# Kernel optimization log

Hardware: AMD Instinct MI355X
Metric: run time of the kernel (lower is better)

## Reference

```python
import jax, jax.numpy as jnp
import numpy as np

DIM, N_HEADS, HEAD_DIM, BASE = 1024, 16, 64, 10000.0
B, S = 2, 2048


def setup_inputs() -> dict:
    key = jax.random.key(0)
    ks = jax.random.split(key, 8)
    theta = (BASE ** (-jnp.arange(0, HEAD_DIM, 2, dtype=jnp.float32) / HEAD_DIM))  # [head_dim//2]
    s = 0.02
    return {
        "x": jax.random.normal(ks[0], (B, S, DIM), jnp.float32),
        "positions": jnp.arange(S, dtype=jnp.int32),
        "theta": theta,
        "Wq": jax.random.normal(ks[1], (DIM, N_HEADS * HEAD_DIM), jnp.float32) * s,
        "bq": jnp.zeros((N_HEADS * HEAD_DIM,), jnp.float32),
        "Wk": jax.random.normal(ks[2], (DIM, N_HEADS * HEAD_DIM), jnp.float32) * s,
        "bk": jnp.zeros((N_HEADS * HEAD_DIM,), jnp.float32),
        "Wv": jax.random.normal(ks[3], (DIM, N_HEADS * HEAD_DIM), jnp.float32) * s,
        "bv": jnp.zeros((N_HEADS * HEAD_DIM,), jnp.float32),
        "Wo": jax.random.normal(ks[4], (N_HEADS * HEAD_DIM, DIM), jnp.float32) * s,
        "bo": jnp.zeros((DIM,), jnp.float32),
    }


def _rope(x, theta):
    # x: [B, H, S, head_dim]; theta: [head_dim//2]
    seq_len = x.shape[2]
    ang = jnp.arange(seq_len, dtype=x.dtype)[:, None] * theta  # [S, head_dim//2]
    cos = jnp.cos(ang)[None, None]  # [1,1,S,head_dim//2]
    sin = jnp.sin(ang)[None, None]
    x1, x2 = x[..., 0::2], x[..., 1::2]
    # matches torch.cat([-x2*sin + x1*cos, x1*sin + x2*cos], dim=-1)
    return jnp.concatenate([x1 * cos - x2 * sin, x1 * sin + x2 * cos], axis=-1)


def reference(x, positions, theta, Wq, bq, Wk, bk, Wv, bv, Wo, bo):
    batch, seq_len, _ = x.shape
    H, hd = N_HEADS, HEAD_DIM

    def split_heads(t):
        return t.reshape(batch, seq_len, H, hd).transpose(0, 2, 1, 3)  # [B,H,S,hd]

    q = split_heads(x @ Wq + bq)
    k = split_heads(x @ Wk + bk)
    v = split_heads(x @ Wv + bv)
    q = _rope(q, theta)
    k = _rope(k, theta)

    scale = 1.0 / jnp.sqrt(jnp.asarray(hd, x.dtype))
    scores = jnp.einsum("bhqd,bhkd->bhqk", q, k) * scale  # [B,H,S,S]
    causal = jnp.tril(jnp.ones((seq_len, seq_len), dtype=bool))
    scores = jnp.where(causal, scores, jnp.asarray(-jnp.inf, x.dtype))
    attn = jax.nn.softmax(scores, axis=-1)  # dropout is identity at eval
    out = jnp.einsum("bhqk,bhkd->bhqd", attn, v)  # [B,H,S,hd]
    out = out.transpose(0, 2, 1, 3).reshape(batch, seq_len, H * hd)
    return out @ Wo + bo
```

## Files before the change

### kernel.cpp

```cpp
#include <hip/hip_runtime.h>
#include <math.h>

#define B_   2
#define S_   2048
#define DIM_ 1024
#define H_   16
#define HD_  64
#define BS_  (B_ * S_)
#define BHSD ((size_t)B_ * H_ * S_ * HD_)
#define CEXP 0.1803368801111244f

typedef unsigned short u16;
typedef unsigned int   u32;
typedef short s16x8 __attribute__((ext_vector_type(8)));
typedef float f32x4 __attribute__((ext_vector_type(4)));

#define MFMA16(a, b, c) __builtin_amdgcn_mfma_f32_16x16x32_bf16((a), (b), (c), 0, 0, 0)

__device__ __forceinline__ u16 f2bf(float f) {
    u32 u = __float_as_uint(f);
    u += 0x7fffu + ((u >> 16) & 1u);
    return (u16)(u >> 16);
}
__device__ __forceinline__ float bf2f(u16 h) {
    return __uint_as_float(((u32)h) << 16);
}
__device__ __forceinline__ u32 cvt_pk_bf16(float a, float b) {
    u32 r;
    asm("v_cvt_pk_bf16_f32 %0, %1, %2" : "=v"(r) : "v"(a), "v"(b));
    return r;
}
__device__ __forceinline__ void gl16(void* lds, const void* g) {
    __builtin_amdgcn_global_load_lds(
        (__attribute__((address_space(1))) void*)(g),
        (__attribute__((address_space(3))) void*)(lds), 16, 0, 0);
}

__global__ __launch_bounds__(256) void prep(
    const float* __restrict__ x, u16* __restrict__ xb,
    const float* __restrict__ W0, const float* __restrict__ W1,
    const float* __restrict__ W2, const float* __restrict__ W3,
    u16* __restrict__ T0, u16* __restrict__ T1,
    u16* __restrict__ T2, u16* __restrict__ T3,
    const float* __restrict__ bq, const float* __restrict__ bk,
    const float* __restrict__ bv, float* __restrict__ bias3,
    const float* __restrict__ theta, float2* __restrict__ cs)
{
    __shared__ float tile[32][33];
    const int bid = blockIdx.x, tid = threadIdx.x;

    if (bid < 2048) {
        const int i = bid * 256 + tid;
        const float4 a = *(const float4*)(x + (size_t)i * 8);
        const float4 b = *(const float4*)(x + (size_t)i * 8 + 4);
        s16x8 o;
        o[0] = (short)f2bf(a.x); o[1] = (short)f2bf(a.y);
        o[2] = (short)f2bf(a.z); o[3] = (short)f2bf(a.w);
        o[4] = (short)f2bf(b.x); o[5] = (short)f2bf(b.y);
        o[6] = (short)f2bf(b.z); o[7] = (short)f2bf(b.w);
        *(s16x8*)(xb + (size_t)i * 8) = o;
    } else if (bid < 6144) {
        const int idx = bid - 2048;
        const int z = idx >> 10;
        const float* W; u16* T;
        switch (z) {
            case 0: W = W0; T = T0; break;
            case 1: W = W1; T = T1; break;
            case 2: W = W2; T = T2; break;
            default: W = W3; T = T3; break;
        }
        const int n0 = ((idx >> 5) & 31) * 32, k0 = (idx & 31) * 32;
        const int c = tid & 31, rr = tid >> 5;
#pragma unroll
        for (int i = 0; i < 4; ++i) {
            const int k = rr + i * 8;
            tile[k][c] = W[(size_t)(k0 + k) * DIM_ + n0 + c];
        }
        __syncthreads();
#pragma unroll
        for (int i = 0; i < 4; ++i) {
            const int col = n0 + rr + i * 8;
            int pcol = col;
            if (z < 2) {
                const int dd = col & 63;
                const int pd = (dd & 1) ? 32 + (dd >> 1) : (dd >> 1);
                pcol = (col & ~63) | pd;
            }
            T[(size_t)pcol * DIM_ + k0 + c] = f2bf(tile[c][rr + i * 8]);
        }
    } else if (bid < 6400) {
        const int idx = bid - 6144;
        const int s = idx * 8 + (tid >> 5), j = tid & 31;
        float sn, cn;
        sincosf((float)s * theta[j], &sn, &cn);
        cs[(s << 5) + j] = make_float2(cn, sn);
    } else {
        const int i = (bid - 6400) * 256 + tid;
        const int which = i >> 10, local = i & 1023;
        const float v = (which == 0) ? bq[local]
                      : (which == 1) ? bk[local] : bv[local];
        int dst = i;
        if (which < 2) {
            const int dd = local & 63;
            const int pd = (dd & 1) ? 32 + (dd >> 1) : (dd >> 1);
            dst = which * 1024 + (local & ~63) + pd;
        }
        bias3[dst] = v;
    }
}

template<int BN, int HMIN, int EPI>
__global__ __launch_bounds__(256, 3) void gemm_mfma(
    const u16* __restrict__ A, const u16* __restrict__ Bt,
    const float* __restrict__ bias, void* __restrict__ Yv,
    const float2* __restrict__ cs)
{
    __shared__ u16 As[128 * 64];
    __shared__ u16 Bs[BN * 64];

    const int tid = threadIdx.x, lane = tid & 63, wid = tid >> 6;
    const int l15 = lane & 15, lg = lane >> 4;
    const int row0 = blockIdx.x * 128, col0 = blockIdx.y * BN;
    const int wr = (wid >> 1) * 64;
    const int wc = (wid & 1) * (BN / 2);
    constexpr int NM = 4, NN = BN / 32, BCH = BN / 32;

    const int l8 = lane >> 3, l7 = lane & 7;
    const int colE = ((l7 ^ l8) << 3);

    const u16* aptr[4]; u16* aldp[4];
#pragma unroll
    for (int i = 0; i < 4; ++i) {
        const int ci = wid * 4 + i;
        const int rr = row0 + ci * 8 + l8;
        size_t a0;
        if (HMIN)
            a0 = (((size_t)(rr >> 11) * H_) * S_ + (rr & (S_ - 1))) * HD_ + colE;
        else
            a0 = (size_t)rr * DIM_ + colE;
        aptr[i] = A + a0;
        aldp[i] = As + ci * 512;
    }
    const u16* bptr[BCH]; u16* bldp[BCH];
#pragma unroll
    for (int i = 0; i < BCH; ++i) {
        const int ci = wid * BCH + i;
        const int rr = col0 + ci * 8 + l8;
        bptr[i] = Bt + (size_t)rr * DIM_ + colE;
        bldp[i] = Bs + ci * 512;
    }
    const size_t astep = HMIN ? (size_t)S_ * HD_ : 64;

    f32x4 acc[NM][NN];
#pragma unroll
    for (int m = 0; m < NM; ++m)
#pragma unroll
        for (int n = 0; n < NN; ++n) acc[m][n] = (f32x4){0.f, 0.f, 0.f, 0.f};

    for (int k0 = 0; k0 < DIM_; k0 += 64) {
        __syncthreads();
#pragma unroll
        for (int i = 0; i < 4; ++i) gl16(aldp[i], aptr[i]);
#pragma unroll
        for (int i = 0; i < BCH; ++i) gl16(bldp[i], bptr[i]);
#pragma unroll
        for (int i = 0; i < 4; ++i) aptr[i] += astep;
#pragma unroll
        for (int i = 0; i < BCH; ++i) bptr[i] += 64;
        __syncthreads();

        s16x8 af[NM][2], bfr[NN][2];
#pragma unroll
        for (int m = 0; m < NM; ++m) {
            const int row = wr + m * 16 + l15;
#pragma unroll
            for (int kf = 0; kf < 2; ++kf)
                af[m][kf] = *(const s16x8*)&As[row * 64 +
                    (((kf * 64 + lg * 16) ^ ((l15 & 7) << 4)) >> 1)];
        }
#pragma unroll
        for (int n = 0; n < NN; ++n) {
            const int row = wc + n * 16 + l15;
#pragma unroll
            for (int kf = 0; kf < 2; ++kf)
                bfr[n][kf] = *(const s16x8*)&Bs[row * 64 +
                    (((kf * 64 + lg * 16) ^ ((l15 & 7) << 4)) >> 1)];
        }
        __builtin_amdgcn_s_setprio(1);
#pragma unroll
        for (int m = 0; m < NM; ++m)
#pragma unroll
            for (int n = 0; n < NN; ++n) {
                acc[m][n] = MFMA16(af[m][0], bfr[n][0], acc[m][n]);
                acc[m][n] = MFMA16(af[m][1], bfr[n][1], acc[m][n]);
            }
        __builtin_amdgcn_s_setprio(0);
    }

    if (EPI == 0) {
        u16* Y = (u16*)Yv;
        const int whichq = (col0 + wc) >> 10;
        if (whichq < 2) {
            const float sclw = (whichq == 0) ? CEXP : 1.0f;
#pragma unroll
            for (int n = 0; n < 2; ++n) {
                const int cc0 = col0 + wc + n * 16 + l15;
                const int j = n * 16 + l15;
                const float bv0 = bias[cc0];
                const float bv1 = bias[cc0 + 32];
                const int hh = (cc0 >> 6) & (H_ - 1);
#pragma unroll
                for (int m = 0; m < NM; ++m)
#pragma unroll
                    for (int r = 0; r < 4; ++r) {
                        const int rr = row0 + wr + m * 16 + lg * 4 + r;
                        const int b = rr >> 11, s = rr & (S_ - 1);
                        const float2 csv = cs[(s << 5) + j];
                        const float v0 = acc[m][n][r] + bv0;
                        const float v1 = acc[m][n + 2][r] + bv1;
                        const size_t base = (size_t)whichq * BHSD
                            + (((size_t)b * H_ + hh) * S_ + s) * HD_;
                        Y[base + j]      = f2bf((v0 * csv.x - v1 * csv.y) * sclw);
                        Y[base + j + 32] = f2bf((v0 * csv.y + v1 * csv.x) * sclw);
                    }
            }
        } else {
#pragma unroll
            for (int n = 0; n < NN; ++n) {
                const int cc = col0 + wc + n * 16 + l15;
                const float bv = bias[cc];
                const int hh = (cc >> 6) & (H_ - 1), d = cc & 63;
#pragma unroll
                for (int m = 0; m < NM; ++m)
#pragma unroll
                    for (int r = 0; r < 4; ++r) {
                        const int rr = row0 + wr + m * 16 + lg * 4 + r;
                        const int b = rr >> 11, s = rr & (S_ - 1);
                        const int sp = (s & ~60) | ((s & 12) << 1)
                                     | ((s & 16) << 1) | ((s & 32) >> 3);
                        Y[2 * BHSD + ((size_t)(b * H_ + hh) * HD_ + d) * S_ + sp] =
                            f2bf(acc[m][n][r] + bv);
                    }
            }
        }
    } else {
#pragma unroll
        for (int n = 0; n < NN; ++n) {
            const int cc = col0 + wc + n * 16 + l15;
            const float bv = bias[cc];
#pragma unroll
            for (int m = 0; m < NM; ++m)
#pragma unroll
                for (int r = 0; r < 4; ++r) {
                    const int rr = row0 + wr + m * 16 + lg * 4 + r;
                    ((float*)Yv)[(size_t)rr * DIM_ + cc] = acc[m][n][r] + bv;
                }
        }
    }
}

__global__ __launch_bounds__(256, 5) void attn_q(
    const u16* __restrict__ Q, const u16* __restrict__ K,
    const u16* __restrict__ VT, u16* __restrict__ Opart,
    float* __restrict__ lpart)
{
    const int bh = blockIdx.x;
    const int y  = blockIdx.y;
    const int a = y >> 4, r0_ = y & 15;
    const int b = r0_ >> 1, half = r0_ & 1;
    const int qt = (a == 0) ? (31 - b) : (a == 1) ? (16 + b)
                 : (a == 2) ? (15 - b) : b;
    const int T = qt + 1, h0 = (T + 1) >> 1;
    const int kvlo = half ? h0 : 0;
    const int kvhi = half ? T : h0;
    const int nst = kvhi - kvlo;

    const u16* Qg = Q + (size_t)bh * S_ * HD_;
    const u16* Kg = K + (size_t)bh * S_ * HD_;
    const u16* Vg = VT + (size_t)bh * HD_ * S_;

    __shared__ u16 Ks[2][64 * 64];
    __shared__ u16 Vs[2][64 * 64];

    const int tid = threadIdx.x;
    const int w = tid >> 6, lane = tid & 63;
    const int q0 = qt * 64 + w * 16;
    const int l15 = lane & 15, lg = lane >> 4;

    const int crow = lane >> 3, cslt = lane & 7;

    auto stage = [&](int bufi, int j0) {
#pragma unroll
        for (int i = 0; i < 2; ++i) {
            const int c = w * 2 + i;
            const int row = c * 8 + crow;
            const int soff = ((cslt ^ (row & 7)) << 3);
            gl16(&Ks[bufi][c * 512], Kg + (size_t)(j0 + row) * HD_ + soff);
            gl16(&Vs[bufi][c * 512], Vg + (size_t)row * S_ + j0 + soff);
        }
    };

    s16x8 qf[2];
    {
        const u16* qrow = Qg + (size_t)(q0 + l15) * HD_ + lg * 8;
        qf[0] = *(const s16x8*)(qrow);
        qf[1] = *(const s16x8*)(qrow + 32);
    }

    s16x8 onesv;
#pragma unroll
    for (int i = 0; i < 8; ++i) onesv[i] = (short)0x3F80;

    f32x4 o[4], ol;
#pragma unroll
    for (int n = 0; n < 4; ++n) o[n] = (f32x4){0.f, 0.f, 0.f, 0.f};
    ol = (f32x4){0.f, 0.f, 0.f, 0.f};

    stage(0, kvlo * 64);
    __syncthreads();

    int buf = 0;
    for (int s = 0; s < nst; ++s) {
        const int t = kvlo + s;
        if (s + 1 < nst) stage(buf ^ 1, (t + 1) * 64);

        const u16* Kb = Ks[buf];
        const u16* Vb = Vs[buf];

        f32x4 sc[4];
        __builtin_amdgcn_s_setprio(1);
#pragma unroll
        for (int sub = 0; sub < 4; ++sub) {
            const int kr = sub * 16 + l15;
            const s16x8 kf0 = *(const s16x8*)&Kb[kr * 64 + ((lg ^ (kr & 7)) << 3)];
            const s16x8 kf1 = *(const s16x8*)&Kb[kr * 64 + (((lg + 4) ^ (kr & 7)) << 3)];
            f32x4 z = (f32x4){0.f, 0.f, 0.f, 0.f};
            z = MFMA16(kf0, qf[0], z);
            sc[sub] = MFMA16(kf1, qf[1], z);
        }
        __builtin_amdgcn_s_setprio(0);

        if (t == qt) {
#pragma unroll
            for (int sub = 0; sub < 4; ++sub) {
                if (sub == w) {
#pragma unroll
                    for (int r = 0; r < 4; ++r)
                        if (lg * 4 + r > l15) sc[sub][r] = -1e30f;
                } else if (sub > w) {
#pragma unroll
                    for (int r = 0; r < 4; ++r) sc[sub][r] = -1e30f;
                }
            }
        }

        float p[4][4];
#pragma unroll
        for (int sub = 0; sub < 4; ++sub)
#pragma unroll
            for (int r = 0; r < 4; ++r)
                p[sub][r] = __builtin_amdgcn_exp2f(sc[sub][r]);

        union { s16x8 v; u32 w4[4]; } af[2];
#pragma unroll
        for (int step = 0; step < 2; ++step)
#pragma unroll
            for (int jj = 0; jj < 4; ++jj) {
                const int sub = (jj >> 1) * 2 + step;
                const int rr0 = (jj & 1) * 2;
                af[step].w4[jj] = cvt_pk_bf16(p[sub][rr0], p[sub][rr0 + 1]);
            }
        __builtin_amdgcn_s_setprio(1);
#pragma unroll
        for (int n = 0; n < 4; ++n) {
            const int d = n * 16 + l15;
            const s16x8 vf0 = *(const s16x8*)&Vb[d * 64 + ((lg ^ (d & 7)) << 3)];
            const s16x8 vf1 = *(const s16x8*)&Vb[d * 64 + (((lg + 4) ^ (d & 7)) << 3)];
            o[n] = MFMA16(af[0].v, vf0, o[n]);
            o[n] = MFMA16(af[1].v, vf1, o[n]);
        }
        ol = MFMA16(af[0].v, onesv, ol);
        ol = MFMA16(af[1].v, onesv, ol);
        __builtin_amdgcn_s_setprio(0);

        __syncthreads();
        buf ^= 1;
    }

    const size_t it = ((size_t)(bh * 32 + qt) * 2 + half);
    u16* op = Opart + it * 4096;
#pragma unroll
    for (int r = 0; r < 4; ++r) {
        const int rowl = w * 16 + lg * 4 + r;
#pragma unroll
        for (int n = 0; n < 4; ++n)
            op[rowl * 64 + n * 16 + l15] = f2bf(o[n][r]);
        if (l15 == 0) lpart[it * 64 + rowl] = ol[r];
    }
}

__global__ __launch_bounds__(256) void attn_merge(
    const u16* __restrict__ Opart, const float* __restrict__ lpart,
    u16* __restrict__ Q)
{
    const int bh = blockIdx.x, qt = blockIdx.y, tid = threadIdx.x;
    const size_t it0 = (size_t)(bh * 32 + qt) * 2;
    const int row = tid >> 2, c0 = (tid & 3) * 16;

    const float l = lpart[it0 * 64 + row] + lpart[(it0 + 1) * 64 + row];
    const float inv = 1.f / l;

    const u16* p0 = Opart + it0 * 4096 + row * 64 + c0;
    const u16* p1 = p0 + 4096;
    u16* dst = Q + ((size_t)bh * S_ + qt * 64 + row) * HD_ + c0;

    const s16x8 a0 = *(const s16x8*)p0,       a1 = *(const s16x8*)p1;
    const s16x8 b0 = *(const s16x8*)(p0 + 8), b1 = *(const s16x8*)(p1 + 8);
    s16x8 oA, oB;
#pragma unroll
    for (int j = 0; j < 8; ++j) {
        oA[j] = (short)f2bf((bf2f((u16)a0[j]) + bf2f((u16)a1[j])) * inv);
        oB[j] = (short)f2bf((bf2f((u16)b0[j]) + bf2f((u16)b1[j])) * inv);
    }
    *(s16x8*)dst = oA;
    *(s16x8*)(dst + 8) = oB;
}

extern "C" void kernel_launch(void* const* d_in, const int* in_sizes, int n_in,
                              void* d_out, int out_size, void* d_ws, size_t ws_size,
                              hipStream_t stream)
{
    (void)in_sizes; (void)n_in; (void)out_size; (void)ws_size;
    const float* x     = (const float*)d_in[0];
    const float* theta = (const float*)d_in[2];
    const float* Wq    = (const float*)d_in[3];
    const float* bq    = (const float*)d_in[4];
    const float* Wk    = (const float*)d_in[5];
    const float* bk    = (const float*)d_in[6];
    const float* Wv    = (const float*)d_in[7];
    const float* bv    = (const float*)d_in[8];
    const float* Wo    = (const float*)d_in[9];
    const float* bo    = (const float*)d_in[10];
    float* out = (float*)d_out;

    u16* xb  = (u16*)d_ws;
    u16* wtq = xb + (size_t)BS_ * DIM_;
    u16* wtk = wtq + (size_t)DIM_ * DIM_;
    u16* wtv = wtk + (size_t)DIM_ * DIM_;
    u16* wto = wtv + (size_t)DIM_ * DIM_;
    u16* qws = wto + (size_t)DIM_ * DIM_;
    u16* kws = qws + BHSD;
    u16* vtw = kws + BHSD;
    float* bias3 = (float*)(vtw + BHSD);
    float2* cs = (float2*)(bias3 + 4096);
    u16* opart = (u16*)(cs + (size_t)S_ * 32);
    float* lpart = (float*)(opart + (size_t)2048 * 4096);

    prep<<<dim3(6412), dim3(256), 0, stream>>>(
        x, xb, Wq, Wk, Wv, Wo, wtq, wtk, wtv, wto, bq, bk, bv, bias3, theta, cs);

    gemm_mfma<128, 0, 0><<<dim3(32, 24), dim3(256), 0, stream>>>(
        xb, wtq, bias3, qws, cs);

    attn_q<<<dim3(32, 64), dim3(256), 0, stream>>>(qws, kws, vtw, opart, lpart);

    attn_merge<<<dim3(32, 32), dim3(256), 0, stream>>>(opart, lpart, qws);

    gemm_mfma<64, 1, 1><<<dim3(32, 16), dim3(256), 0, stream>>>(
        qws, wto, bo, out, cs);
}
```

Measured before the change: 91.93 us.

## Fuse split-KV attention merge into output projection GEMM A-tile load

Removes the separate attn_merge kernel by having the output-projection GEMM load both partial attention outputs and their softmax sums, normalise and convert to bf16, and write the A tile straight into shared memory. The template GEMM is split into a dedicated QKV kernel and a dedicated o-proj kernel. This saves one launch plus a write and re-read of the merged attention output. In exchange, A loads become synchronous register loads with conversion math instead of async global-to-LDS copies, and each A element is read from two partial buffers. Every o-proj column block repeats that merge work.

```diff
diff --git a/kernel.cpp b/kernel.cpp
--- a/kernel.cpp
+++ b/kernel.cpp
@@ -109,21 +109,20 @@
     }
 }
 
-template<int BN, int HMIN, int EPI>
-__global__ __launch_bounds__(256, 3) void gemm_mfma(
+__global__ __launch_bounds__(256, 3) void gemm_qkv(
     const u16* __restrict__ A, const u16* __restrict__ Bt,
-    const float* __restrict__ bias, void* __restrict__ Yv,
+    const float* __restrict__ bias, u16* __restrict__ Y,
     const float2* __restrict__ cs)
 {
     __shared__ u16 As[128 * 64];
-    __shared__ u16 Bs[BN * 64];
+    __shared__ u16 Bs[128 * 64];
 
     const int tid = threadIdx.x, lane = tid & 63, wid = tid >> 6;
     const int l15 = lane & 15, lg = lane >> 4;
-    const int row0 = blockIdx.x * 128, col0 = blockIdx.y * BN;
+    const int row0 = blockIdx.x * 128, col0 = blockIdx.y * 128;
     const int wr = (wid >> 1) * 64;
-    const int wc = (wid & 1) * (BN / 2);
-    constexpr int NM = 4, NN = BN / 32, BCH = BN / 32;
+    const int wc = (wid & 1) * 64;
+    constexpr int NM = 4, NN = 4, BCH = 4;
 
     const int l8 = lane >> 3, l7 = lane & 7;
     const int colE = ((l7 ^ l8) << 3);
@@ -132,24 +131,16 @@
 #pragma unroll
     for (int i = 0; i < 4; ++i) {
         const int ci = wid * 4 + i;
-        const int rr = row0 + ci * 8 + l8;
-        size_t a0;
-        if (HMIN)
-            a0 = (((size_t)(rr >> 11) * H_) * S_ + (rr & (S_ - 1))) * HD_ + colE;
-        else
-            a0 = (size_t)rr * DIM_ + colE;
-        aptr[i] = A + a0;
+        aptr[i] = A + (size_t)(row0 + ci * 8 + l8) * DIM_ + colE;
         aldp[i] = As + ci * 512;
     }
     const u16* bptr[BCH]; u16* bldp[BCH];
 #pragma unroll
     for (int i = 0; i < BCH; ++i) {
         const int ci = wid * BCH + i;
-        const int rr = col0 + ci * 8 + l8;
-        bptr[i] = Bt + (size_t)rr * DIM_ + colE;
+        bptr[i] = Bt + (size_t)(col0 + ci * 8 + l8) * DIM_ + colE;
         bldp[i] = Bs + ci * 512;
     }
-    const size_t astep = HMIN ? (size_t)S_ * HD_ : 64;
 
     f32x4 acc[NM][NN];
 #pragma unroll
@@ -164,7 +155,7 @@
 #pragma unroll
         for (int i = 0; i < BCH; ++i) gl16(bldp[i], bptr[i]);
 #pragma unroll
-        for (int i = 0; i < 4; ++i) aptr[i] += astep;
+        for (int i = 0; i < 4; ++i) aptr[i] += 64;
 #pragma unroll
         for (int i = 0; i < BCH; ++i) bptr[i] += 64;
         __syncthreads();
@@ -197,63 +188,47 @@
         __builtin_amdgcn_s_setprio(0);
     }
 
-    if (EPI == 0) {
-        u16* Y = (u16*)Yv;
-        const int whichq = (col0 + wc) >> 10;
-        if (whichq < 2) {
-            const float sclw = (whichq == 0) ? CEXP : 1.0f;
-#pragma unroll
-            for (int n = 0; n < 2; ++n) {
-                const int cc0 = col0 + wc + n * 16 + l15;
-                const int j = n * 16 + l15;
-                const float bv0 = bias[cc0];
-                const float bv1 = bias[cc0 + 32];
-                const int hh = (cc0 >> 6) & (H_ - 1);
-#pragma unroll
-                for (int m = 0; m < NM; ++m)
-#pragma unroll
-                    for (int r = 0; r < 4; ++r) {
-                        const int rr = row0 + wr + m * 16 + lg * 4 + r;
-                        const int b = rr >> 11, s = rr & (S_ - 1);
-                        const float2 csv = cs[(s << 5) + j];
-                        const float v0 = acc[m][n][r] + bv0;
-                        const float v1 = acc[m][n + 2][r] + bv1;
-                        const size_t base = (size_t)whichq * BHSD
-                            + (((size_t)b * H_ + hh) * S_ + s) * HD_;
-                        Y[base + j]      = f2bf((v0 * csv.x - v1 * csv.y) * sclw);
-                        Y[base + j + 32] = f2bf((v0 * csv.y + v1 * csv.x) * sclw);
-                    }
-            }
-        } else {
-#pragma unroll
-            for (int n = 0; n < NN; ++n) {
-                const int cc = col0 + wc + n * 16 + l15;
-                const float bv = bias[cc];
-                const int hh = (cc >> 6) & (H_ - 1), d = cc & 63;
-#pragma unroll
-                for (int m = 0; m < NM; ++m)
-#pragma unroll
-                    for (int r = 0; r < 4; ++r) {
-                        const int rr = row0 + wr + m * 16 + lg * 4 + r;
-                        const int b = rr >> 11, s = rr & (S_ - 1);
-                        const int sp = (s & ~60) | ((s & 12) << 1)
-                                     | ((s & 16) << 1) | ((s & 32) >> 3);
-                        Y[2 * BHSD + ((size_t)(b * H_ + hh) * HD_ + d) * S_ + sp] =
-                            f2bf(acc[m][n][r] + bv);
-                    }
-            }
+    const int whichq = (col0 + wc) >> 10;
+    if (whichq < 2) {
+        const float sclw = (whichq == 0) ? CEXP : 1.0f;
+#pragma unroll
+        for (int n = 0; n < 2; ++n) {
+            const int cc0 = col0 + wc + n * 16 + l15;
+            const int j = n * 16 + l15;
+            const float bv0 = bias[cc0];
+            const float bv1 = bias[cc0 + 32];
+            const int hh = (cc0 >> 6) & (H_ - 1);
+#pragma unroll
+            for (int m = 0; m < NM; ++m)
+#pragma unroll
+                for (int r = 0; r < 4; ++r) {
+                    const int rr = row0 + wr + m * 16 + lg * 4 + r;
+                    const int b = rr >> 11, s = rr & (S_ - 1);
+                    const float2 csv = cs[(s << 5) + j];
+                    const float v0 = acc[m][n][r] + bv0;
+                    const float v1 = acc[m][n + 2][r] + bv1;
+                    const size_t base = (size_t)whichq * BHSD
+                        + (((size_t)b * H_ + hh) * S_ + s) * HD_;
+                    Y[base + j]      = f2bf((v0 * csv.x - v1 * csv.y) * sclw);
+                    Y[base + j + 32] = f2bf((v0 * csv.y + v1 * csv.x) * sclw);
+                }
         }
     } else {
 #pragma unroll
         for (int n = 0; n < NN; ++n) {
             const int cc = col0 + wc + n * 16 + l15;
             const float bv = bias[cc];
+            const int hh = (cc >> 6) & (H_ - 1), d = cc & 63;
 #pragma unroll
             for (int m = 0; m < NM; ++m)
 #pragma unroll
                 for (int r = 0; r < 4; ++r) {
                     const int rr = row0 + wr + m * 16 + lg * 4 + r;
-                    ((float*)Yv)[(size_t)rr * DIM_ + cc] = acc[m][n][r] + bv;
+                    const int b = rr >> 11, s = rr & (S_ - 1);
+                    const int sp = (s & ~60) | ((s & 12) << 1)
+                                 | ((s & 16) << 1) | ((s & 32) >> 3);
+                    Y[2 * BHSD + ((size_t)(b * H_ + hh) * HD_ + d) * S_ + sp] =
+                        f2bf(acc[m][n][r] + bv);
                 }
         }
     }
@@ -399,31 +374,115 @@
     }
 }
 
-__global__ __launch_bounds__(256) void attn_merge(
+__global__ __launch_bounds__(256, 3) void gemm_oproj(
     const u16* __restrict__ Opart, const float* __restrict__ lpart,
-    u16* __restrict__ Q)
+    const u16* __restrict__ Bt, const float* __restrict__ bias,
+    float* __restrict__ Y)
 {
-    const int bh = blockIdx.x, qt = blockIdx.y, tid = threadIdx.x;
-    const size_t it0 = (size_t)(bh * 32 + qt) * 2;
-    const int row = tid >> 2, c0 = (tid & 3) * 16;
-
-    const float l = lpart[it0 * 64 + row] + lpart[(it0 + 1) * 64 + row];
-    const float inv = 1.f / l;
-
-    const u16* p0 = Opart + it0 * 4096 + row * 64 + c0;
-    const u16* p1 = p0 + 4096;
-    u16* dst = Q + ((size_t)bh * S_ + qt * 64 + row) * HD_ + c0;
-
-    const s16x8 a0 = *(const s16x8*)p0,       a1 = *(const s16x8*)p1;
-    const s16x8 b0 = *(const s16x8*)(p0 + 8), b1 = *(const s16x8*)(p1 + 8);
-    s16x8 oA, oB;
-#pragma unroll
-    for (int j = 0; j < 8; ++j) {
-        oA[j] = (short)f2bf((bf2f((u16)a0[j]) + bf2f((u16)a1[j])) * inv);
-        oB[j] = (short)f2bf((bf2f((u16)b0[j]) + bf2f((u16)b1[j])) * inv);
-    }
-    *(s16x8*)dst = oA;
-    *(s16x8*)(dst + 8) = oB;
+    __shared__ u16 As[128 * 64];
+    __shared__ u16 Bs[64 * 64];
+
+    const int tid = threadIdx.x, lane = tid & 63, wid = tid >> 6;
+    const int l15 = lane & 15, lg = lane >> 4;
+    const int row0 = blockIdx.x * 128, col0 = blockIdx.y * 64;
+    const int wr = (wid >> 1) * 64;
+    const int wc = (wid & 1) * 32;
+
+    const int l8 = lane >> 3, l7 = lane & 7;
+    const int colE = ((l7 ^ l8) << 3);
+
+    int base_[4], rowl_[4];
+#pragma unroll
+    for (int i = 0; i < 4; ++i) {
+        const int ci = wid * 4 + i;
+        const int rr = row0 + ci * 8 + l8;
+        const int b = rr >> 11, s = rr & (S_ - 1);
+        base_[i] = b * 1024 + (s >> 6) * 2;
+        rowl_[i] = s & 63;
+    }
+    const u16* bptr[2]; u16* bldp[2];
+#pragma unroll
+    for (int i = 0; i < 2; ++i) {
+        const int ci = wid * 2 + i;
+        bptr[i] = Bt + (size_t)(col0 + ci * 8 + l8) * DIM_ + colE;
+        bldp[i] = Bs + ci * 512;
+    }
+
+    f32x4 acc[4][2];
+#pragma unroll
+    for (int m = 0; m < 4; ++m)
+#pragma unroll
+        for (int n = 0; n < 2; ++n) acc[m][n] = (f32x4){0.f, 0.f, 0.f, 0.f};
+
+    for (int k0 = 0; k0 < DIM_; k0 += 64) {
+        const int h = k0 >> 6;
+        __syncthreads();
+#pragma unroll
+        for (int i = 0; i < 2; ++i) gl16(bldp[i], bptr[i]);
+#pragma unroll
+        for (int i = 0; i < 2; ++i) bptr[i] += 64;
+
+#pragma unroll
+        for (int i = 0; i < 4; ++i) {
+            const int it0 = base_[i] + h * 64;
+            const u16* p0 = Opart + (size_t)it0 * 4096 + rowl_[i] * 64 + colE;
+            const s16x8 a0 = *(const s16x8*)p0;
+            const s16x8 a1 = *(const s16x8*)(p0 + 4096);
+            const float lsum = lpart[it0 * 64 + rowl_[i]]
+                             + lpart[it0 * 64 + 64 + rowl_[i]];
+            const float inv = __builtin_amdgcn_rcpf(lsum);
+            union { s16x8 v; u32 w4[4]; } am;
+#pragma unroll
+            for (int j = 0; j < 4; ++j) {
+                const float v0 = (bf2f((u16)a0[2 * j])     + bf2f((u16)a1[2 * j]))     * inv;
+                const float v1 = (bf2f((u16)a0[2 * j + 1]) + bf2f((u16)a1[2 * j + 1])) * inv;
+                am.w4[j] = cvt_pk_bf16(v0, v1);
+            }
+            const int ci = wid * 4 + i;
+            *(s16x8*)&As[ci * 512 + lane * 8] = am.v;
+        }
+        __syncthreads();
+
+        s16x8 af[4][2], bfr[2][2];
+#pragma unroll
+        for (int m = 0; m < 4; ++m) {
+            const int row = wr + m * 16 + l15;
+#pragma unroll
+            for (int kf = 0; kf < 2; ++kf)
+                af[m][kf] = *(const s16x8*)&As[row * 64 +
+                    (((kf * 64 + lg * 16) ^ ((l15 & 7) << 4)) >> 1)];
+        }
+#pragma unroll
+        for (int n = 0; n < 2; ++n) {
+            const int row = wc + n * 16 + l15;
+#pragma unroll
+            for (int kf = 0; kf < 2; ++kf)
+                bfr[n][kf] = *(const s16x8*)&Bs[row * 64 +
+                    (((kf * 64 + lg * 16) ^ ((l15 & 7) << 4)) >> 1)];
+        }
+        __builtin_amdgcn_s_setprio(1);
+#pragma unroll
+        for (int m = 0; m < 4; ++m)
+#pragma unroll
+            for (int n = 0; n < 2; ++n) {
+                acc[m][n] = MFMA16(af[m][0], bfr[n][0], acc[m][n]);
+                acc[m][n] = MFMA16(af[m][1], bfr[n][1], acc[m][n]);
+            }
+        __builtin_amdgcn_s_setprio(0);
+    }
+
+#pragma unroll
+    for (int n = 0; n < 2; ++n) {
+        const int cc = col0 + wc + n * 16 + l15;
+        const float bv = bias[cc];
+#pragma unroll
+        for (int m = 0; m < 4; ++m)
+#pragma unroll
+            for (int r = 0; r < 4; ++r) {
+                const int rr = row0 + wr + m * 16 + lg * 4 + r;
+                Y[(size_t)rr * DIM_ + cc] = acc[m][n][r] + bv;
+            }
+    }
 }
 
 extern "C" void kernel_launch(void* const* d_in, const int* in_sizes, int n_in,
@@ -459,13 +518,10 @@
     prep<<<dim3(6412), dim3(256), 0, stream>>>(
         x, xb, Wq, Wk, Wv, Wo, wtq, wtk, wtv, wto, bq, bk, bv, bias3, theta, cs);
 
-    gemm_mfma<128, 0, 0><<<dim3(32, 24), dim3(256), 0, stream>>>(
-        xb, wtq, bias3, qws, cs);
+    gemm_qkv<<<dim3(32, 24), dim3(256), 0, stream>>>(xb, wtq, bias3, qws, cs);
 
     attn_q<<<dim3(32, 64), dim3(256), 0, stream>>>(qws, kws, vtw, opart, lpart);
 
-    attn_merge<<<dim3(32, 32), dim3(256), 0, stream>>>(opart, lpart, qws);
-
-    gemm_mfma<64, 1, 1><<<dim3(32, 16), dim3(256), 0, stream>>>(
-        qws, wto, bo, out, cs);
-}
+    gemm_oproj<<<dim3(32, 16), dim3(256), 0, stream>>>(
+        opart, lpart, wto, bo, out);
+}
```

Result: slower. 107.4 us (+16.8%).
